# Kernel optimization log

Hardware: AMD Instinct MI355X
Metric: run time of the kernel (lower is better)

Reference implementation:

```python
import jax, jax.numpy as jnp
import numpy as np

O, D, E, K, H, A = 1024, 1024, 16, 4, 2048, 64  # option_dim, obs_dim, num_experts, k, moe_hidden, act_dim
LOSS_COEF = 0.01


def cv_squared(x):
    # torch .var() is unbiased (ddof=1)
    eps = 1e-10
    return jnp.var(x, ddof=1) / (jnp.mean(x) ** 2 + eps)


def setup_inputs() -> dict:
    key = jax.random.key(0)
    ks = jax.random.split(key, 8)
    s = 0.02
    return {
        "obs": jax.random.normal(ks[0], (O, D), jnp.float32),
        # original inits w_gate to zeros (degenerate top-k); use small random for a meaningful baseline
        "w_gate": jax.random.normal(ks[1], (O, D, E), jnp.float32) * s,
        "w1": jax.random.normal(ks[2], (E, D, H), jnp.float32) * s,   # expert MLP layer 1
        "b1": jnp.zeros((E, H), jnp.float32),
        "w2": jax.random.normal(ks[3], (E, H, A), jnp.float32) * s,   # expert MLP layer 2
        "b2": jnp.zeros((E, A), jnp.float32),
        "last_w": jax.random.normal(ks[4], (O, D, A), jnp.float32),   # last_w_layer
        "last_b": jax.random.normal(ks[5], (O, A), jnp.float32),      # last_b_layer
    }


def reference(obs, w_gate, w1, b1, w2, b2, last_w, last_b):
    # ---- noisy_top_k_gating (this version applies no noise) ----
    logits = jnp.einsum('od,ode->oe', obs, w_gate)                    # [O, E]
    top_vals, top_idx = jax.lax.top_k(logits, K + 1)
    topk_gates = jax.nn.softmax(top_vals[:, :K], axis=1)              # softmax over top-k logits
    rows = jnp.arange(O)[:, None]
    gates = jnp.zeros_like(logits).at[rows, top_idx[:, :K]].set(topk_gates)  # scatter -> [O, E]
    importance = gates.sum(axis=1)
    load = (gates > 0).sum(axis=1).astype(jnp.float32)                # faithful to original (sum over dim 1)
    loss = (cv_squared(importance) + cv_squared(load)) * LOSS_COEF
    # ---- dispatch / expert MLPs / combine (dense-over-experts equivalent; zero gates kill non-top-k) ----
    h = jax.nn.relu(jnp.einsum('od,edh->oeh', obs, w1) + b1[None])    # [O, E, H]
    y = jnp.einsum('oe,oeh,eha->oa', gates, h, w2) + gates @ b2       # [O, A]
    # ---- action head ----
    mu = jnp.einsum('od,oda->oa', obs, last_w) + last_b               # [O, A]
    action_probs = jax.nn.softmax(mu, axis=-1)
    z = (action_probs == 0.0).astype(action_probs.dtype) * 1e-08
    log_action_probs = jnp.log(action_probs + z)
    return (action_probs, log_action_probs, y, loss)
```

## Files before the change

kernel.cpp:

```cpp
#include <hip/hip_runtime.h>
#include <hip/hip_bf16.h>
#include <math.h>

#define O_ 1024
#define D_ 1024
#define E_ 16
#define K_ 4
#define H_ 2048
#define A_ 64
#define LOSS_COEF 0.01f

#define FLT_MIN_NORMAL 1.17549435e-38f

using floatx4 = __attribute__((ext_vector_type(4))) float;
using fragb   = __attribute__((ext_vector_type(8))) short;

static __device__ __forceinline__ ushort f2bf(float f) {
    unsigned u = __builtin_bit_cast(unsigned, f);
    u += 0x7fffu + ((u >> 16) & 1u);
    return (ushort)(u >> 16);
}

static __device__ __forceinline__ void gld_lds16(const void* g, void* l) {
    __builtin_amdgcn_global_load_lds(
        (const __attribute__((address_space(1))) void*)g,
        (__attribute__((address_space(3))) void*)l, 16, 0, 0);
}

__global__ __launch_bounds__(256) void prep_kernel(
    const float* __restrict__ w1, const float* __restrict__ w2,
    ushort* __restrict__ w1T, ushort* __restrict__ w2T, int* __restrict__ cnt)
{
    const int bid = blockIdx.x;
    if (bid == 0) {
        if (threadIdx.x < E_) cnt[threadIdx.x] = 0;
        return;
    }
    int id = bid - 1;
    const float* src; ushort* dst; int R, C, c0, r0, e;
    if (id < 8192) {
        c0 = (id & 31) * 64; r0 = ((id >> 5) & 15) * 64; e = id >> 9;
        src = w1; dst = w1T; R = D_; C = H_;
    } else {
        id -= 8192;
        c0 = 0; r0 = (id & 31) * 64; e = id >> 5;
        src = w2; dst = w2T; R = H_; C = A_;
    }

    __shared__ ushort tile[64][72];
    const float* s = src + (size_t)e * R * C;
    const int t = threadIdx.x;
    const int rr = t >> 4, cq = t & 15;
    #pragma unroll
    for (int i = 0; i < 4; ++i) {
        int r = rr + i * 16;
        float4 v = *(const float4*)(s + (size_t)(r0 + r) * C + c0 + cq * 4);
        ushort4 u;
        u.x = f2bf(v.x); u.y = f2bf(v.y); u.z = f2bf(v.z); u.w = f2bf(v.w);
        *(ushort4*)&tile[r][cq * 4] = u;
    }
    __syncthreads();
    ushort* dbase = dst + (size_t)e * R * C;
    const int cc = t >> 4, rq = t & 15;
    #pragma unroll
    for (int i = 0; i < 4; ++i) {
        int c = cc + i * 16;
        ushort4 u;
        u.x = tile[rq * 4 + 0][c];
        u.y = tile[rq * 4 + 1][c];
        u.z = tile[rq * 4 + 2][c];
        u.w = tile[rq * 4 + 3][c];
        *(ushort4*)(dbase + (size_t)(c0 + c) * R + r0 + rq * 4) = u;
    }
}

__global__ __launch_bounds__(256) void gating_kernel(
    const float* __restrict__ obs, const float* __restrict__ w_gate,
    const float* __restrict__ b2,
    int* __restrict__ cnt, int* __restrict__ rows, float* __restrict__ gatev,
    float* __restrict__ imp, float* __restrict__ loadv,
    ushort* __restrict__ obs_bf, float* __restrict__ yout)
{
    const int o = blockIdx.x;
    const int t = threadIdx.x;
    __shared__ float xs[D_];
    __shared__ float part[64][20];
    __shared__ float logits[E_];
    __shared__ int   sidx[K_];
    __shared__ float sgate[K_];

    const float4* xrow = (const float4*)(obs + (size_t)o * D_);
    for (int i = t; i < D_ / 4; i += 256) ((float4*)xs)[i] = xrow[i];
    __syncthreads();

    const int dg = t >> 2, e4 = t & 3;
    const float4* wg = (const float4*)(w_gate + (size_t)o * (D_ * E_));
    float4 acc = make_float4(0.f, 0.f, 0.f, 0.f);
    #pragma unroll 4
    for (int i = 0; i < 16; ++i) {
        int d = dg + (i << 6);
        float4 w = wg[d * 4 + e4];
        float x = xs[d];
        acc.x += x * w.x; acc.y += x * w.y; acc.z += x * w.z; acc.w += x * w.w;
    }
    *(float4*)&part[dg][e4 * 4] = acc;
    __syncthreads();
    if (t < E_) {
        float s = 0.f;
        for (int g = 0; g < 64; ++g) s += part[g][t];
        logits[t] = s;
    }
    __syncthreads();
    if (t == 0) {
        float lv[E_];
        #pragma unroll
        for (int i = 0; i < E_; ++i) lv[i] = logits[i];
        int idx[K_]; float val[K_];
        bool used[E_] = {};
        for (int k = 0; k < K_; ++k) {
            int bi = 0; float bv = -INFINITY;
            for (int i = 0; i < E_; ++i)
                if (!used[i] && lv[i] > bv) { bv = lv[i]; bi = i; }
            used[bi] = true; idx[k] = bi; val[k] = bv;
        }
        float m = val[0];
        float ex[K_]; float s = 0.f;
        for (int k = 0; k < K_; ++k) { ex[k] = expf(val[k] - m); s += ex[k]; }
        float inv = 1.f / s;
        float sumg = 0.f; int ld = 0;
        for (int k = 0; k < K_; ++k) {
            float g = ex[k] * inv;
            sidx[k] = idx[k]; sgate[k] = g;
            int pos = atomicAdd(&cnt[idx[k]], 1);
            rows[idx[k] * O_ + pos]  = o;
            gatev[idx[k] * O_ + pos] = g;
            sumg += g;
            if (g > 0.f) ld++;
        }
        imp[o] = sumg;
        loadv[o] = (float)ld;
    }

    {
        float4 v = ((const float4*)xs)[t];
        ushort4 u;
        u.x = f2bf(v.x); u.y = f2bf(v.y); u.z = f2bf(v.z); u.w = f2bf(v.w);
        ((ushort4*)(obs_bf + (size_t)o * D_))[t] = u;
    }
    __syncthreads();

    if (t < A_) {
        float accy = 0.f;
        #pragma unroll
        for (int k = 0; k < K_; ++k)
            accy += sgate[k] * b2[sidx[k] * A_ + t];
        yout[(size_t)o * A_ + t] = accy;
    }
}

__global__ __launch_bounds__(256, 2) void mega_kernel(
    const ushort* __restrict__ obs_bf, const ushort* __restrict__ w1T,
    const float* __restrict__ b1, const ushort* __restrict__ w2T,
    const int* __restrict__ cnt, const int* __restrict__ rows,
    const float* __restrict__ gatev, float* __restrict__ y,
    const float* __restrict__ obs, const float* __restrict__ last_w,
    const float* __restrict__ last_b,
    float* __restrict__ probs, float* __restrict__ logprobs,
    const float* __restrict__ imp, const float* __restrict__ loadv,
    float* __restrict__ out_loss)
{
    const int bid = blockIdx.x;
    const int t = threadIdx.x;

    __shared__ __align__(16) ushort smem[32768];
    __shared__ int   rid_s[128];
    __shared__ float rgate_s[128];
    __shared__ float b1s[128];
    __shared__ float xs[D_];
    __shared__ float red[16][A_];
    __shared__ float ls1[256], ls2[256];
    __shared__ float mean1, mean2;

    if (bid == 0) {
        float a[4], b[4];
        float pa = 0.f, pb = 0.f;
        #pragma unroll
        for (int j = 0; j < 4; ++j) {
            a[j] = imp[t + 256 * j]; b[j] = loadv[t + 256 * j];
            pa += a[j]; pb += b[j];
        }
        ls1[t] = pa; ls2[t] = pb; __syncthreads();
        for (int s = 128; s > 0; s >>= 1) {
            if (t < s) { ls1[t] += ls1[t + s]; ls2[t] += ls2[t + s]; }
            __syncthreads();
        }
        if (t == 0) { mean1 = ls1[0] / O_; mean2 = ls2[0] / O_; }
        __syncthreads();
        pa = 0.f; pb = 0.f;
        #pragma unroll
        for (int j = 0; j < 4; ++j) {
            float d1 = a[j] - mean1, d2 = b[j] - mean2;
            pa += d1 * d1; pb += d2 * d2;
        }
        ls1[t] = pa; ls2[t] = pb; __syncthreads();
        for (int s = 128; s > 0; s >>= 1) {
            if (t < s) { ls1[t] += ls1[t + s]; ls2[t] += ls2[t + s]; }
            __syncthreads();
        }
        if (t == 0) {
            float var1 = ls1[0] / (O_ - 1), var2 = ls2[0] / (O_ - 1);
            const float eps = 1e-10f;
            out_loss[0] = (var1 / (mean1 * mean1 + eps) + var2 / (mean2 * mean2 + eps)) * LOSS_COEF;
        }
        return;
    }

    if (bid <= 2048) {
        const int id = bid - 1;
        const int ht = id & 15, rt = (id >> 4) & 7, e = id >> 7;
        const int n = cnt[e];
        if (rt * 128 >= n) return;

        const int wv = t >> 6, l = t & 63;
        const int lm = l & 15, q = l >> 4;
        const int wr = wv >> 1, wc = wv & 1;

        if (t < 128) {
            int gi = rt * 128 + t;
            rid_s[t]   = (gi < n) ? rows[e * O_ + gi]  : -1;
            rgate_s[t] = (gi < n) ? gatev[e * O_ + gi] : 0.f;
        } else {
            b1s[t - 128] = b1[e * H_ + ht * 128 + (t - 128)];
        }
        __syncthreads();

        const int swe = ((l & 7) ^ (l >> 3)) << 3;
        const ushort* asrc[4];
        const ushort* bsrc[4];
        #pragma unroll
        for (int j = 0; j < 4; ++j) {
            int r = (j * 4 + wv) * 8 + (l >> 3);
            int arow = rid_s[r]; if (arow < 0) arow = 0;
            asrc[j] = obs_bf + (size_t)arow * D_ + swe;
            bsrc[j] = w1T + ((size_t)(e * H_ + ht * 128 + r)) * D_ + swe;
        }

        auto stage = [&](int b, int kc) {
            ushort* ab_ = &smem[b * 8192];
            ushort* bb_ = &smem[16384 + b * 8192];
            const int ko = kc * 64;
            #pragma unroll
            for (int j = 0; j < 4; ++j) {
                gld_lds16(asrc[j] + ko, ab_ + (j * 4 + wv) * 512);
                gld_lds16(bsrc[j] + ko, bb_ + (j * 4 + wv) * 512);
            }
        };

        floatx4 acc[4][4] = {};
        int buf = 0;
        stage(0, 0);
        __syncthreads();

        for (int kc = 0; kc < 16; ++kc) {
            if (kc < 15) stage(buf ^ 1, kc + 1);
            const ushort* ab = &smem[buf * 8192];
            const ushort* bb = &smem[16384 + buf * 8192];
            #pragma unroll
            for (int ks = 0; ks < 2; ++ks) {
                const int co = ((ks * 4 + q) ^ (lm & 7)) << 3;
                fragb a[4];
                #pragma unroll
                for (int i = 0; i < 4; ++i)
                    a[i] = *(const fragb*)(ab + (wr * 64 + i * 16 + lm) * 64 + co);
                #pragma unroll
                for (int nt = 0; nt < 4; ++nt) {
                    fragb b = *(const fragb*)(bb + (wc * 64 + nt * 16 + lm) * 64 + co);
                    #pragma unroll
                    for (int i = 0; i < 4; ++i)
                        acc[i][nt] = __builtin_amdgcn_mfma_f32_16x16x32_bf16(a[i], b, acc[i][nt], 0, 0, 0);
                }
            }
            __syncthreads();
            buf ^= 1;
        }

        ushort* Hs = smem;
        #pragma unroll
        for (int i = 0; i < 4; ++i) {
            #pragma unroll
            for (int nt = 0; nt < 4; ++nt) {
                const int col = wc * 64 + nt * 16 + lm;
                const float bb = b1s[col];
                #pragma unroll
                for (int r = 0; r < 4; ++r) {
                    const int row = wr * 64 + i * 16 + q * 4 + r;
                    float h = acc[i][nt][r] + bb;
                    h = h > 0.f ? h : 0.f;
                    Hs[row * 136 + col] = f2bf(h * rgate_s[row]);
                }
            }
        }
        __syncthreads();

        floatx4 acc2[4][2] = {};
        #pragma unroll
        for (int ks = 0; ks < 4; ++ks) {
            fragb a[4];
            #pragma unroll
            for (int i = 0; i < 4; ++i)
                a[i] = *(const fragb*)(Hs + (wr * 64 + i * 16 + lm) * 136 + ks * 32 + q * 8);
            #pragma unroll
            for (int nt = 0; nt < 2; ++nt) {
                const int acol = wc * 32 + nt * 16 + lm;
                fragb b = *(const fragb*)(w2T + ((size_t)(e * A_ + acol)) * H_ + ht * 128 + ks * 32 + q * 8);
                #pragma unroll
                for (int i = 0; i < 4; ++i)
                    acc2[i][nt] = __builtin_amdgcn_mfma_f32_16x16x32_bf16(a[i], b, acc2[i][nt], 0, 0, 0);
            }
        }

        #pragma unroll
        for (int i = 0; i < 4; ++i) {
            #pragma unroll
            for (int r = 0; r < 4; ++r) {
                const int row = wr * 64 + i * 16 + q * 4 + r;
                const int orow = rid_s[row];
                if (orow >= 0) {
                    #pragma unroll
                    for (int nt = 0; nt < 2; ++nt)
                        atomicAdd(&y[(size_t)orow * A_ + wc * 32 + nt * 16 + lm], acc2[i][nt][r]);
                }
            }
        }
        return;
    }

    {
        const int o = bid - 2049;

        const float4* xrow = (const float4*)(obs + (size_t)o * D_);
        for (int i = t; i < D_ / 4; i += 256) ((float4*)xs)[i] = xrow[i];
        __syncthreads();

        const int a4 = t & 15, dg = t >> 4;
        const float* lw = last_w + (size_t)o * (D_ * A_);
        float acc0 = 0.f, acc1 = 0.f, acc2 = 0.f, acc3 = 0.f;
        #pragma unroll 8
        for (int i = 0; i < D_ / 16; ++i) {
            int d = dg + (i << 4);
            float4 w = *(const float4*)(lw + (size_t)d * A_ + a4 * 4);
            float x = xs[d];
            acc0 += x * w.x; acc1 += x * w.y; acc2 += x * w.z; acc3 += x * w.w;
        }
        *(float4*)&red[dg][a4 * 4] = make_float4(acc0, acc1, acc2, acc3);
        __syncthreads();

        if (t < A_) {
            float mu = last_b[(size_t)o * A_ + t];
            #pragma unroll
            for (int g = 0; g < 16; ++g) mu += red[g][t];
            float mx = mu;
            #pragma unroll
            for (int off = 32; off > 0; off >>= 1) mx = fmaxf(mx, __shfl_xor(mx, off, 64));
            float ex = expf(mu - mx);
            if (ex < FLT_MIN_NORMAL) ex = 0.f;
            float s = ex;
            #pragma unroll
            for (int off = 32; off > 0; off >>= 1) s += __shfl_xor(s, off, 64);
            float p = ex / s;
            if (p < FLT_MIN_NORMAL) p = 0.f;
            probs[(size_t)o * A_ + t] = p;
            float z = (p == 0.f) ? 1e-8f : 0.f;
            logprobs[(size_t)o * A_ + t] = logf(p + z);
        }
    }
}

extern "C" void kernel_launch(void* const* d_in, const int* in_sizes, int n_in,
                              void* d_out, int out_size, void* d_ws, size_t ws_size,
                              hipStream_t stream)
{
    const float* obs    = (const float*)d_in[0];
    const float* w_gate = (const float*)d_in[1];
    const float* w1     = (const float*)d_in[2];
    const float* b1     = (const float*)d_in[3];
    const float* w2     = (const float*)d_in[4];
    const float* b2     = (const float*)d_in[5];
    const float* last_w = (const float*)d_in[6];
    const float* last_b = (const float*)d_in[7];

    float* out   = (float*)d_out;
    float* probs = out;
    float* logp  = out + O_ * A_;
    float* yout  = out + 2 * O_ * A_;
    float* loss  = out + 3 * O_ * A_;

    char* ws = (char*)d_ws;
    float*  imp       = (float*)(ws + (32 << 10));
    float*  loadv     = (float*)(ws + (36 << 10));
    int*    cnt       = (int*)(ws + (40 << 10));
    int*    rows      = (int*)(ws + (41 << 10));
    float*  gatev     = (float*)(ws + (105 << 10));
    ushort* obs_bf    = (ushort*)(ws + (256 << 10));
    ushort* w1T       = (ushort*)(ws + (256 << 10) + (2 << 20));
    ushort* w2T       = (ushort*)(ws + (256 << 10) + (66 << 20));

    hipLaunchKernelGGL(prep_kernel, dim3(1 + 8192 + 512), dim3(256), 0, stream,
                       w1, w2, w1T, w2T, cnt);
    hipLaunchKernelGGL(gating_kernel, dim3(O_), dim3(256), 0, stream,
                       obs, w_gate, b2, cnt, rows, gatev, imp, loadv, obs_bf, yout);
    hipLaunchKernelGGL(mega_kernel, dim3(1 + 2048 + 1024), dim3(256), 0, stream,
                       obs_bf, w1T, b1, w2T, cnt, rows, gatev, yout,
                       obs, last_w, last_b, probs, logp, imp, loadv, loss);
}
```

Measured before the change: 569.8 us.

## Merge prep and gating kernels, single-buffer expert GEMM for higher occupancy, remap blocks

Folds the weight transpose/convert and the gating pass into one front kernel so the two run side by side, and clears the expert counters with a memset. In the main kernel, LDS use is cut by dropping the double buffer and aliasing scratch arrays into shared memory, and launch bounds go from 2 to 4 blocks per CU. Expert-GEMM block indices are remapped so that tiles of the same expert row are spread across XCDs. The price is losing load/compute overlap in the K loop, which now waits on a barrier after every stage.

```diff
diff --git a/kernel.cpp b/kernel.cpp
--- a/kernel.cpp
+++ b/kernel.cpp
@@ -27,138 +27,137 @@
         (__attribute__((address_space(3))) void*)l, 16, 0, 0);
 }
 
-__global__ __launch_bounds__(256) void prep_kernel(
+__global__ __launch_bounds__(256) void front_kernel(
+    const float* __restrict__ obs, const float* __restrict__ w_gate,
+    const float* __restrict__ b2,
     const float* __restrict__ w1, const float* __restrict__ w2,
-    ushort* __restrict__ w1T, ushort* __restrict__ w2T, int* __restrict__ cnt)
+    int* __restrict__ cnt, int* __restrict__ rows, float* __restrict__ gatev,
+    float* __restrict__ imp, float* __restrict__ loadv,
+    ushort* __restrict__ obs_bf, float* __restrict__ yout,
+    ushort* __restrict__ w1T, ushort* __restrict__ w2T)
 {
     const int bid = blockIdx.x;
-    if (bid == 0) {
-        if (threadIdx.x < E_) cnt[threadIdx.x] = 0;
+    const int t = threadIdx.x;
+    __shared__ __align__(16) char sh[9344];
+
+    if (bid < 1024) {
+        const int o = bid;
+        float* xs            = (float*)sh;
+        float (*part)[20]    = (float(*)[20])(sh + 4096);
+        float* logits        = (float*)(sh + 9216);
+        int*   sidx          = (int*)(sh + 9280);
+        float* sgate         = (float*)(sh + 9296);
+
+        const float4* xrow = (const float4*)(obs + (size_t)o * D_);
+        for (int i = t; i < D_ / 4; i += 256) ((float4*)xs)[i] = xrow[i];
+        __syncthreads();
+
+        const int dg = t >> 2, e4 = t & 3;
+        const float4* wg = (const float4*)(w_gate + (size_t)o * (D_ * E_));
+        float4 acc = make_float4(0.f, 0.f, 0.f, 0.f);
+        #pragma unroll 4
+        for (int i = 0; i < 16; ++i) {
+            int d = dg + (i << 6);
+            float4 w = wg[d * 4 + e4];
+            float x = xs[d];
+            acc.x += x * w.x; acc.y += x * w.y; acc.z += x * w.z; acc.w += x * w.w;
+        }
+        *(float4*)&part[dg][e4 * 4] = acc;
+        __syncthreads();
+        if (t < E_) {
+            float s = 0.f;
+            for (int g = 0; g < 64; ++g) s += part[g][t];
+            logits[t] = s;
+        }
+        __syncthreads();
+        if (t == 0) {
+            float lv[E_];
+            #pragma unroll
+            for (int i = 0; i < E_; ++i) lv[i] = logits[i];
+            int idx[K_]; float val[K_];
+            bool used[E_] = {};
+            for (int k = 0; k < K_; ++k) {
+                int bi = 0; float bv = -INFINITY;
+                for (int i = 0; i < E_; ++i)
+                    if (!used[i] && lv[i] > bv) { bv = lv[i]; bi = i; }
+                used[bi] = true; idx[k] = bi; val[k] = bv;
+            }
+            float m = val[0];
+            float ex[K_]; float s = 0.f;
+            for (int k = 0; k < K_; ++k) { ex[k] = expf(val[k] - m); s += ex[k]; }
+            float inv = 1.f / s;
+            float sumg = 0.f; int ld = 0;
+            for (int k = 0; k < K_; ++k) {
+                float g = ex[k] * inv;
+                sidx[k] = idx[k]; sgate[k] = g;
+                int pos = atomicAdd(&cnt[idx[k]], 1);
+                rows[idx[k] * O_ + pos]  = o;
+                gatev[idx[k] * O_ + pos] = g;
+                sumg += g;
+                if (g > 0.f) ld++;
+            }
+            imp[o] = sumg;
+            loadv[o] = (float)ld;
+        }
+
+        {
+            float4 v = ((const float4*)xs)[t];
+            ushort4 u;
+            u.x = f2bf(v.x); u.y = f2bf(v.y); u.z = f2bf(v.z); u.w = f2bf(v.w);
+            ((ushort4*)(obs_bf + (size_t)o * D_))[t] = u;
+        }
+        __syncthreads();
+
+        if (t < A_) {
+            float accy = 0.f;
+            #pragma unroll
+            for (int k = 0; k < K_; ++k)
+                accy += sgate[k] * b2[sidx[k] * A_ + t];
+            yout[(size_t)o * A_ + t] = accy;
+        }
         return;
     }
-    int id = bid - 1;
-    const float* src; ushort* dst; int R, C, c0, r0, e;
-    if (id < 8192) {
-        c0 = (id & 31) * 64; r0 = ((id >> 5) & 15) * 64; e = id >> 9;
-        src = w1; dst = w1T; R = D_; C = H_;
-    } else {
-        id -= 8192;
-        c0 = 0; r0 = (id & 31) * 64; e = id >> 5;
-        src = w2; dst = w2T; R = H_; C = A_;
-    }
-
-    __shared__ ushort tile[64][72];
-    const float* s = src + (size_t)e * R * C;
-    const int t = threadIdx.x;
-    const int rr = t >> 4, cq = t & 15;
-    #pragma unroll
-    for (int i = 0; i < 4; ++i) {
-        int r = rr + i * 16;
-        float4 v = *(const float4*)(s + (size_t)(r0 + r) * C + c0 + cq * 4);
-        ushort4 u;
-        u.x = f2bf(v.x); u.y = f2bf(v.y); u.z = f2bf(v.z); u.w = f2bf(v.w);
-        *(ushort4*)&tile[r][cq * 4] = u;
-    }
-    __syncthreads();
-    ushort* dbase = dst + (size_t)e * R * C;
-    const int cc = t >> 4, rq = t & 15;
-    #pragma unroll
-    for (int i = 0; i < 4; ++i) {
-        int c = cc + i * 16;
-        ushort4 u;
-        u.x = tile[rq * 4 + 0][c];
-        u.y = tile[rq * 4 + 1][c];
-        u.z = tile[rq * 4 + 2][c];
-        u.w = tile[rq * 4 + 3][c];
-        *(ushort4*)(dbase + (size_t)(c0 + c) * R + r0 + rq * 4) = u;
+
+    {
+        int id = bid - 1024;
+        const float* src; ushort* dst; int R, C, c0, r0, e;
+        if (id < 8192) {
+            c0 = (id & 31) * 64; r0 = ((id >> 5) & 15) * 64; e = id >> 9;
+            src = w1; dst = w1T; R = D_; C = H_;
+        } else {
+            id -= 8192;
+            c0 = 0; r0 = (id & 31) * 64; e = id >> 5;
+            src = w2; dst = w2T; R = H_; C = A_;
+        }
+
+        ushort (*tile)[72] = (ushort(*)[72])sh;
+        const float* s = src + (size_t)e * R * C;
+        const int rr = t >> 4, cq = t & 15;
+        #pragma unroll
+        for (int i = 0; i < 4; ++i) {
+            int r = rr + i * 16;
+            float4 v = *(const float4*)(s + (size_t)(r0 + r) * C + c0 + cq * 4);
+            ushort4 u;
+            u.x = f2bf(v.x); u.y = f2bf(v.y); u.z = f2bf(v.z); u.w = f2bf(v.w);
+            *(ushort4*)&tile[r][cq * 4] = u;
+        }
+        __syncthreads();
+        ushort* dbase = dst + (size_t)e * R * C;
+        const int cc = t >> 4, rq = t & 15;
+        #pragma unroll
+        for (int i = 0; i < 4; ++i) {
+            int c = cc + i * 16;
+            ushort4 u;
+            u.x = tile[rq * 4 + 0][c];
+            u.y = tile[rq * 4 + 1][c];
+            u.z = tile[rq * 4 + 2][c];
+            u.w = tile[rq * 4 + 3][c];
+            *(ushort4*)(dbase + (size_t)(c0 + c) * R + r0 + rq * 4) = u;
+        }
     }
 }
 
-__global__ __launch_bounds__(256) void gating_kernel(
-    const float* __restrict__ obs, const float* __restrict__ w_gate,
-    const float* __restrict__ b2,
-    int* __restrict__ cnt, int* __restrict__ rows, float* __restrict__ gatev,
-    float* __restrict__ imp, float* __restrict__ loadv,
-    ushort* __restrict__ obs_bf, float* __restrict__ yout)
-{
-    const int o = blockIdx.x;
-    const int t = threadIdx.x;
-    __shared__ float xs[D_];
-    __shared__ float part[64][20];
-    __shared__ float logits[E_];
-    __shared__ int   sidx[K_];
-    __shared__ float sgate[K_];
-
-    const float4* xrow = (const float4*)(obs + (size_t)o * D_);
-    for (int i = t; i < D_ / 4; i += 256) ((float4*)xs)[i] = xrow[i];
-    __syncthreads();
-
-    const int dg = t >> 2, e4 = t & 3;
-    const float4* wg = (const float4*)(w_gate + (size_t)o * (D_ * E_));
-    float4 acc = make_float4(0.f, 0.f, 0.f, 0.f);
-    #pragma unroll 4
-    for (int i = 0; i < 16; ++i) {
-        int d = dg + (i << 6);
-        float4 w = wg[d * 4 + e4];
-        float x = xs[d];
-        acc.x += x * w.x; acc.y += x * w.y; acc.z += x * w.z; acc.w += x * w.w;
-    }
-    *(float4*)&part[dg][e4 * 4] = acc;
-    __syncthreads();
-    if (t < E_) {
-        float s = 0.f;
-        for (int g = 0; g < 64; ++g) s += part[g][t];
-        logits[t] = s;
-    }
-    __syncthreads();
-    if (t == 0) {
-        float lv[E_];
-        #pragma unroll
-        for (int i = 0; i < E_; ++i) lv[i] = logits[i];
-        int idx[K_]; float val[K_];
-        bool used[E_] = {};
-        for (int k = 0; k < K_; ++k) {
-            int bi = 0; float bv = -INFINITY;
-            for (int i = 0; i < E_; ++i)
-                if (!used[i] && lv[i] > bv) { bv = lv[i]; bi = i; }
-            used[bi] = true; idx[k] = bi; val[k] = bv;
-        }
-        float m = val[0];
-        float ex[K_]; float s = 0.f;
-        for (int k = 0; k < K_; ++k) { ex[k] = expf(val[k] - m); s += ex[k]; }
-        float inv = 1.f / s;
-        float sumg = 0.f; int ld = 0;
-        for (int k = 0; k < K_; ++k) {
-            float g = ex[k] * inv;
-            sidx[k] = idx[k]; sgate[k] = g;
-            int pos = atomicAdd(&cnt[idx[k]], 1);
-            rows[idx[k] * O_ + pos]  = o;
-            gatev[idx[k] * O_ + pos] = g;
-            sumg += g;
-            if (g > 0.f) ld++;
-        }
-        imp[o] = sumg;
-        loadv[o] = (float)ld;
-    }
-
-    {
-        float4 v = ((const float4*)xs)[t];
-        ushort4 u;
-        u.x = f2bf(v.x); u.y = f2bf(v.y); u.z = f2bf(v.z); u.w = f2bf(v.w);
-        ((ushort4*)(obs_bf + (size_t)o * D_))[t] = u;
-    }
-    __syncthreads();
-
-    if (t < A_) {
-        float accy = 0.f;
-        #pragma unroll
-        for (int k = 0; k < K_; ++k)
-            accy += sgate[k] * b2[sidx[k] * A_ + t];
-        yout[(size_t)o * A_ + t] = accy;
-    }
-}
-
-__global__ __launch_bounds__(256, 2) void mega_kernel(
+__global__ __launch_bounds__(256, 4) void mega_kernel(
     const ushort* __restrict__ obs_bf, const ushort* __restrict__ w1T,
     const float* __restrict__ b1, const ushort* __restrict__ w2T,
     const int* __restrict__ cnt, const int* __restrict__ rows,
@@ -172,16 +171,15 @@
     const int bid = blockIdx.x;
     const int t = threadIdx.x;
 
-    __shared__ __align__(16) ushort smem[32768];
+    __shared__ __align__(16) ushort smem[17408];
     __shared__ int   rid_s[128];
     __shared__ float rgate_s[128];
     __shared__ float b1s[128];
-    __shared__ float xs[D_];
-    __shared__ float red[16][A_];
-    __shared__ float ls1[256], ls2[256];
     __shared__ float mean1, mean2;
 
     if (bid == 0) {
+        float* ls1 = (float*)smem;
+        float* ls2 = ls1 + 256;
         float a[4], b[4];
         float pa = 0.f, pb = 0.f;
         #pragma unroll
@@ -216,8 +214,12 @@
     }
 
     if (bid <= 2048) {
-        const int id = bid - 1;
-        const int ht = id & 15, rt = (id >> 4) & 7, e = id >> 7;
+        const int id  = bid - 1;
+        const int xcd = id & 7;
+        const int r8  = (id >> 3) & 7;
+        const int phi = id >> 6;
+        const int p   = (phi << 3) | xcd;
+        const int e   = p >> 4, ht = p & 15, rt = r8;
         const int n = cnt[e];
         if (rt * 128 >= n) return;
 
@@ -245,9 +247,9 @@
             bsrc[j] = w1T + ((size_t)(e * H_ + ht * 128 + r)) * D_ + swe;
         }
 
-        auto stage = [&](int b, int kc) {
-            ushort* ab_ = &smem[b * 8192];
-            ushort* bb_ = &smem[16384 + b * 8192];
+        auto stage = [&](int kc) {
+            ushort* ab_ = &smem[0];
+            ushort* bb_ = &smem[8192];
             const int ko = kc * 64;
             #pragma unroll
             for (int j = 0; j < 4; ++j) {
@@ -257,14 +259,11 @@
         };
 
         floatx4 acc[4][4] = {};
-        int buf = 0;
-        stage(0, 0);
-        __syncthreads();
-
+        const ushort* ab = &smem[0];
+        const ushort* bb = &smem[8192];
         for (int kc = 0; kc < 16; ++kc) {
-            if (kc < 15) stage(buf ^ 1, kc + 1);
-            const ushort* ab = &smem[buf * 8192];
-            const ushort* bb = &smem[16384 + buf * 8192];
+            stage(kc);
+            __syncthreads();
             #pragma unroll
             for (int ks = 0; ks < 2; ++ks) {
                 const int co = ((ks * 4 + q) ^ (lm & 7)) << 3;
@@ -281,7 +280,6 @@
                 }
             }
             __syncthreads();
-            buf ^= 1;
         }
 
         ushort* Hs = smem;
@@ -290,11 +288,11 @@
             #pragma unroll
             for (int nt = 0; nt < 4; ++nt) {
                 const int col = wc * 64 + nt * 16 + lm;
-                const float bb = b1s[col];
+                const float bb2 = b1s[col];
                 #pragma unroll
                 for (int r = 0; r < 4; ++r) {
                     const int row = wr * 64 + i * 16 + q * 4 + r;
-                    float h = acc[i][nt][r] + bb;
+                    float h = acc[i][nt][r] + bb2;
                     h = h > 0.f ? h : 0.f;
                     Hs[row * 136 + col] = f2bf(h * rgate_s[row]);
                 }
@@ -337,6 +335,8 @@
 
     {
         const int o = bid - 2049;
+        float* xs = (float*)smem;
+        float (*red)[A_] = (float(*)[A_])(smem + 2048);
 
         const float4* xrow = (const float4*)(obs + (size_t)o * D_);
         for (int i = t; i < D_ / 4; i += 256) ((float4*)xs)[i] = xrow[i];
@@ -405,10 +405,11 @@
     ushort* w1T       = (ushort*)(ws + (256 << 10) + (2 << 20));
     ushort* w2T       = (ushort*)(ws + (256 << 10) + (66 << 20));
 
-    hipLaunchKernelGGL(prep_kernel, dim3(1 + 8192 + 512), dim3(256), 0, stream,
-                       w1, w2, w1T, w2T, cnt);
-    hipLaunchKernelGGL(gating_kernel, dim3(O_), dim3(256), 0, stream,
-                       obs, w_gate, b2, cnt, rows, gatev, imp, loadv, obs_bf, yout);
+    hipMemsetAsync(cnt, 0, E_ * sizeof(int), stream);
+
+    hipLaunchKernelGGL(front_kernel, dim3(1024 + 8192 + 512), dim3(256), 0, stream,
+                       obs, w_gate, b2, w1, w2,
+                       cnt, rows, gatev, imp, loadv, obs_bf, yout, w1T, w2T);
     hipLaunchKernelGGL(mega_kernel, dim3(1 + 2048 + 1024), dim3(256), 0, stream,
                        obs_bf, w1T, b1, w2T, cnt, rows, gatev, yout,
                        obs, last_w, last_b, probs, logp, imp, loadv, loss);
```

New measurement: 553.1 us. 1.03x faster.
